# Optimization experiments

Hardware: AMD Instinct MI355X
Metric: run time of the kernel (lower is better)

The kernel has to match this reference:

```python
import jax, jax.numpy as jnp
import numpy as np

EPS = 1e-12
ETA = 1.0


def _l2norm(x, eps=EPS):
    # torch F.normalize: x / max(||x||, eps)
    n = jnp.sqrt(jnp.sum(x * x, axis=-1, keepdims=True))
    return x / jnp.maximum(n, eps)


def setup_inputs() -> dict:
    key = jax.random.key(0)
    ks = jax.random.split(key, 7)
    B, IN, H = 256, 512, 512
    std = 1.0 / np.sqrt(H)
    return {
        "inputs": jax.random.normal(ks[0], (B, IN), jnp.float32),
        "hidden": jax.random.normal(ks[1], (B, H), jnp.float32),
        "assoc_mem": jax.random.normal(ks[2], (B, H, H), jnp.float32),
        "W_ih": jax.random.uniform(ks[3], (3 * H, IN), jnp.float32, -std, std),
        "b_ih": jax.random.uniform(ks[4], (3 * H,), jnp.float32, -std, std),
        "W_hh": jax.random.uniform(ks[5], (3 * H, H), jnp.float32, -std, std),
        "b_hh": jax.random.uniform(ks[6], (3 * H,), jnp.float32, -std, std),
    }


def reference(inputs, hidden, assoc_mem, W_ih, b_ih, W_hh, b_hh):
    H = hidden.shape[-1]
    # projections = ih(inputs) + hh(hidden)  -> [B, 3H]
    proj = inputs @ W_ih.T + b_ih + hidden @ W_hh.T + b_hh
    u_gate, r, x_emb = jnp.split(proj, 3, axis=1)

    # rotation_operator(x_emb, r): Householder-style rotation in span{u, v}
    u = _l2norm(x_emb)                                    # [B, H]
    r_n = _l2norm(r)
    costh = jnp.sum(u * r_n, axis=-1, keepdims=True)      # [B, 1]
    sinth = jnp.sqrt(1.0 - costh ** 2)                    # [B, 1]
    v = _l2norm(r - jnp.sum(u * r, axis=-1, keepdims=True) * u)

    # R = I - uu^T - vv^T + tmp^T Rth tmp
    #   = I + (cos-1)(uu^T + vv^T) + sin (v u^T - u v^T)
    uu = jnp.einsum('bi,bj->bij', u, u)
    vv = jnp.einsum('bi,bj->bij', v, v)
    cross = jnp.einsum('bi,bj->bij', v, u) - jnp.einsum('bi,bj->bij', u, v)
    R = (jnp.eye(H, dtype=hidden.dtype)
         + (costh - 1.0)[..., None] * (uu + vv)
         + sinth[..., None] * cross)                      # [B, H, H]

    # Rth = assoc_mem @ R ; hidden_new = Rth @ hidden
    Rth_full = jnp.einsum('bij,bjk->bik', assoc_mem, R)
    hidden_new = jnp.einsum('bij,bj->bi', Rth_full, hidden)

    c = jax.nn.relu(hidden_new + x_emb)
    new_h = u_gate * hidden + (1.0 - u_gate) * c
    new_h = _l2norm(new_h) * ETA
    return new_h
```

## Files before the change

kernel.cpp:

```cpp
#include <hip/hip_runtime.h>


#define EPSF 1e-12f

__device__ __forceinline__ float block_reduce_sum(float v, float* sbuf) {
#pragma unroll
    for (int off = 32; off >= 1; off >>= 1)
        v += __shfl_xor(v, off, 64);
    const int t = threadIdx.x;
    __syncthreads();
    if ((t & 63) == 0) sbuf[t >> 6] = v;
    __syncthreads();
    return sbuf[0] + sbuf[1] + sbuf[2] + sbuf[3];
}

#define BM 32
#define BN 64
#define BK 32
#define XS_STRIDE (BM + 2)

__global__ __launch_bounds__(256) void gemm_proj(
    const float* __restrict__ inp, const float* __restrict__ hid,
    const float* __restrict__ W_ih, const float* __restrict__ W_hh,
    const float* __restrict__ b_ih, const float* __restrict__ b_hh,
    float* __restrict__ proj)
{
    __shared__ float Xs[BK * XS_STRIDE];
    __shared__ float Ws[BK * BN];
    const int t  = threadIdx.x;
    const int tx = t & 15;
    const int ty = t >> 4;
    const int col0 = blockIdx.x * BN;
    const int row0 = blockIdx.y * BM;

    const int lr = t >> 3;
    const int lk = (t & 7) * 4;

    float acc[2][4] = {};

#pragma unroll
    for (int phase = 0; phase < 2; ++phase) {
        const float* Xg = phase ? hid : inp;
        const float* Wg = phase ? W_hh : W_ih;
        for (int k0 = 0; k0 < 512; k0 += BK) {
            float4 xv  = *(const float4*)(Xg + (size_t)(row0 + lr) * 512 + k0 + lk);
            float4 wv0 = *(const float4*)(Wg + (size_t)(col0 + lr) * 512 + k0 + lk);
            float4 wv1 = *(const float4*)(Wg + (size_t)(col0 + lr + 32) * 512 + k0 + lk);
            __syncthreads();
            Xs[(lk + 0) * XS_STRIDE + lr] = xv.x;
            Xs[(lk + 1) * XS_STRIDE + lr] = xv.y;
            Xs[(lk + 2) * XS_STRIDE + lr] = xv.z;
            Xs[(lk + 3) * XS_STRIDE + lr] = xv.w;
            Ws[(lk + 0) * BN + lr] = wv0.x;
            Ws[(lk + 1) * BN + lr] = wv0.y;
            Ws[(lk + 2) * BN + lr] = wv0.z;
            Ws[(lk + 3) * BN + lr] = wv0.w;
            Ws[(lk + 0) * BN + lr + 32] = wv1.x;
            Ws[(lk + 1) * BN + lr + 32] = wv1.y;
            Ws[(lk + 2) * BN + lr + 32] = wv1.z;
            Ws[(lk + 3) * BN + lr + 32] = wv1.w;
            __syncthreads();
#pragma unroll
            for (int kk = 0; kk < BK; ++kk) {
                float2 xv2 = *(const float2*)&Xs[kk * XS_STRIDE + 2 * ty];
                float4 wv4 = *(const float4*)&Ws[kk * BN + 4 * tx];
                acc[0][0] += xv2.x * wv4.x;
                acc[0][1] += xv2.x * wv4.y;
                acc[0][2] += xv2.x * wv4.z;
                acc[0][3] += xv2.x * wv4.w;
                acc[1][0] += xv2.y * wv4.x;
                acc[1][1] += xv2.y * wv4.y;
                acc[1][2] += xv2.y * wv4.z;
                acc[1][3] += xv2.y * wv4.w;
            }
        }
    }

    const float4 bi = *(const float4*)(b_ih + col0 + 4 * tx);
    const float4 bh = *(const float4*)(b_hh + col0 + 4 * tx);
    const float4 bias = { bi.x + bh.x, bi.y + bh.y, bi.z + bh.z, bi.w + bh.w };
#pragma unroll
    for (int i = 0; i < 2; ++i) {
        const int r = row0 + 2 * ty + i;
        float4 o = { acc[i][0] + bias.x, acc[i][1] + bias.y,
                     acc[i][2] + bias.z, acc[i][3] + bias.w };
        *(float4*)(proj + (size_t)r * 1536 + col0 + 4 * tx) = o;
    }
}

__global__ __launch_bounds__(256) void rotate_kernel(
    const float* __restrict__ proj, const float* __restrict__ hid,
    float* __restrict__ Rh)
{
    __shared__ float sbuf[4];
    const int b = blockIdx.x;
    const int t = threadIdx.x;
    const int j = 2 * t;
    const float* prow = proj + (size_t)b * 1536;
    const float2 x2 = *(const float2*)(prow + 1024 + j);
    const float2 r2 = *(const float2*)(prow + 512 + j);
    const float2 h2 = *(const float2*)(hid + (size_t)b * 512 + j);

    float sx2 = block_reduce_sum(x2.x * x2.x + x2.y * x2.y, sbuf);
    float sr2 = block_reduce_sum(r2.x * r2.x + r2.y * r2.y, sbuf);
    float sxr = block_reduce_sum(x2.x * r2.x + x2.y * r2.y, sbuf);
    float sxh = block_reduce_sum(x2.x * h2.x + x2.y * h2.y, sbuf);

    const float nx = fmaxf(sqrtf(sx2), EPSF);
    const float nr = fmaxf(sqrtf(sr2), EPSF);
    const float costh = sxr / (nx * nr);
    const float sinth = sqrtf(fmaxf(1.0f - costh * costh, 0.0f));
    const float dot_ur = sxr / nx;
    const float a = sxh / nx;

    const float ux = x2.x / nx, uy = x2.y / nx;
    const float wx = r2.x - dot_ur * ux, wy = r2.y - dot_ur * uy;

    float sw2 = block_reduce_sum(wx * wx + wy * wy, sbuf);
    float swh = block_reduce_sum(wx * h2.x + wy * h2.y, sbuf);
    const float nw = fmaxf(sqrtf(sw2), EPSF);
    const float bb = swh / nw;

    const float cm1 = costh - 1.0f;
    const float vx = wx / nw, vy = wy / nw;
    float2 o;
    o.x = h2.x + cm1 * (a * ux + bb * vx) + sinth * (a * vx - bb * ux);
    o.y = h2.y + cm1 * (a * uy + bb * vy) + sinth * (a * vy - bb * uy);
    *(float2*)(Rh + (size_t)b * 512 + j) = o;
}

__global__ __launch_bounds__(256) void matvec_kernel(
    const float* __restrict__ A, const float* __restrict__ Rh,
    float* __restrict__ hn)
{
    __shared__ float Rhs[512];
    const int b = blockIdx.y;
    const int g = blockIdx.x;
    const int t = threadIdx.x;
    *(float2*)(Rhs + 2 * t) = *(const float2*)(Rh + (size_t)b * 512 + 2 * t);
    __syncthreads();
    const int wave = t >> 6, lane = t & 63;
    const float4* Rhs4 = (const float4*)Rhs;
    const float4 x0 = Rhs4[lane];
    const float4 x1 = Rhs4[64 + lane];
    float res = 0.0f;
#pragma unroll 4
    for (int rr = 0; rr < 16; ++rr) {
        const int i = g * 64 + wave * 16 + rr;
        const float4* Arow = (const float4*)(A + ((size_t)b * 512 + i) * 512);
        const float4 a0 = Arow[lane];
        const float4 a1 = Arow[64 + lane];
        float acc = a0.x * x0.x + a0.y * x0.y + a0.z * x0.z + a0.w * x0.w
                  + a1.x * x1.x + a1.y * x1.y + a1.z * x1.z + a1.w * x1.w;
#pragma unroll
        for (int off = 32; off >= 1; off >>= 1)
            acc += __shfl_xor(acc, off, 64);
        if (lane == rr) res = acc;
    }
    if (lane < 16)
        hn[(size_t)b * 512 + g * 64 + wave * 16 + lane] = res;
}

__global__ __launch_bounds__(256) void epilogue_kernel(
    const float* __restrict__ proj, const float* __restrict__ hid,
    const float* __restrict__ hn, float* __restrict__ out)
{
    __shared__ float sbuf[4];
    const int b = blockIdx.x;
    const int t = threadIdx.x;
    const int j = 2 * t;
    const float* prow = proj + (size_t)b * 1536;
    const float2 ug = *(const float2*)(prow + j);
    const float2 xe = *(const float2*)(prow + 1024 + j);
    const float2 h2 = *(const float2*)(hid + (size_t)b * 512 + j);
    const float2 hv = *(const float2*)(hn + (size_t)b * 512 + j);

    const float cx = fmaxf(hv.x + xe.x, 0.0f);
    const float cy = fmaxf(hv.y + xe.y, 0.0f);
    const float tx_ = ug.x * h2.x + (1.0f - ug.x) * cx;
    const float ty_ = ug.y * h2.y + (1.0f - ug.y) * cy;

    const float s = block_reduce_sum(tx_ * tx_ + ty_ * ty_, sbuf);
    const float inv = 1.0f / fmaxf(sqrtf(s), EPSF);
    float2 o = { tx_ * inv, ty_ * inv };
    *(float2*)(out + (size_t)b * 512 + j) = o;
}

extern "C" void kernel_launch(void* const* d_in, const int* in_sizes, int n_in,
                              void* d_out, int out_size, void* d_ws, size_t ws_size,
                              hipStream_t stream)
{
    const float* inp  = (const float*)d_in[0];
    const float* hid  = (const float*)d_in[1];
    const float* A    = (const float*)d_in[2];
    const float* W_ih = (const float*)d_in[3];
    const float* b_ih = (const float*)d_in[4];
    const float* W_hh = (const float*)d_in[5];
    const float* b_hh = (const float*)d_in[6];
    float* out = (float*)d_out;

    float* proj = (float*)d_ws;
    float* Rh   = proj + 256 * 1536;
    float* hn   = Rh + 256 * 512;

    gemm_proj<<<dim3(24, 8), 256, 0, stream>>>(inp, hid, W_ih, W_hh, b_ih, b_hh, proj);
    rotate_kernel<<<dim3(256), 256, 0, stream>>>(proj, hid, Rh);
    matvec_kernel<<<dim3(8, 256), 256, 0, stream>>>(A, Rh, hn);
    epilogue_kernel<<<dim3(256), 256, 0, stream>>>(proj, hid, hn, out);
}
```

Measured before the change: 423.6 us.

## Fuse rotate, matvec and epilogue into one per-batch kernel; prefetch GEMM tiles

Merges the rotation, the batched matrix-vector product over assoc_mem and the normalisation epilogue into a single 1024-thread block per batch row. Rh and hn now stay in shared memory, and the six scalar block reductions are packed into float4 reductions. The matvec reads A with nontemporal loads and 16-lane row groups. The projection GEMM also register-prefetches the next K tile before the compute loop. This removes two launches and the global round-trips of Rh and hn, but only 256 blocks stream the 256 MB matrix, which may limit memory-level parallelism compared with the 2048-block matvec.

Result: faster. 385.8 us (-8.9%).

```diff
diff --git a/kernel.cpp b/kernel.cpp
--- a/kernel.cpp
+++ b/kernel.cpp
@@ -3,21 +3,7 @@
 
 #define EPSF 1e-12f
 
-__device__ __forceinline__ float block_reduce_sum(float v, float* sbuf) {
-#pragma unroll
-    for (int off = 32; off >= 1; off >>= 1)
-        v += __shfl_xor(v, off, 64);
-    const int t = threadIdx.x;
-    __syncthreads();
-    if ((t & 63) == 0) sbuf[t >> 6] = v;
-    __syncthreads();
-    return sbuf[0] + sbuf[1] + sbuf[2] + sbuf[3];
-}
-
-#define BM 32
-#define BN 64
-#define BK 32
-#define XS_STRIDE (BM + 2)
+typedef float vfloat4 __attribute__((ext_vector_type(4)));
 
 __global__ __launch_bounds__(256) void gemm_proj(
     const float* __restrict__ inp, const float* __restrict__ hid,
@@ -25,54 +11,58 @@
     const float* __restrict__ b_ih, const float* __restrict__ b_hh,
     float* __restrict__ proj)
 {
-    __shared__ float Xs[BK * XS_STRIDE];
-    __shared__ float Ws[BK * BN];
+    __shared__ float Xs[32 * 34];
+    __shared__ float Ws[32 * 64];
     const int t  = threadIdx.x;
     const int tx = t & 15;
     const int ty = t >> 4;
-    const int col0 = blockIdx.x * BN;
-    const int row0 = blockIdx.y * BM;
-
+    const int col0 = blockIdx.x * 64;
+    const int row0 = blockIdx.y * 32;
     const int lr = t >> 3;
     const int lk = (t & 7) * 4;
 
     float acc[2][4] = {};
 
-#pragma unroll
-    for (int phase = 0; phase < 2; ++phase) {
-        const float* Xg = phase ? hid : inp;
-        const float* Wg = phase ? W_hh : W_ih;
-        for (int k0 = 0; k0 < 512; k0 += BK) {
-            float4 xv  = *(const float4*)(Xg + (size_t)(row0 + lr) * 512 + k0 + lk);
-            float4 wv0 = *(const float4*)(Wg + (size_t)(col0 + lr) * 512 + k0 + lk);
-            float4 wv1 = *(const float4*)(Wg + (size_t)(col0 + lr + 32) * 512 + k0 + lk);
-            __syncthreads();
-            Xs[(lk + 0) * XS_STRIDE + lr] = xv.x;
-            Xs[(lk + 1) * XS_STRIDE + lr] = xv.y;
-            Xs[(lk + 2) * XS_STRIDE + lr] = xv.z;
-            Xs[(lk + 3) * XS_STRIDE + lr] = xv.w;
-            Ws[(lk + 0) * BN + lr] = wv0.x;
-            Ws[(lk + 1) * BN + lr] = wv0.y;
-            Ws[(lk + 2) * BN + lr] = wv0.z;
-            Ws[(lk + 3) * BN + lr] = wv0.w;
-            Ws[(lk + 0) * BN + lr + 32] = wv1.x;
-            Ws[(lk + 1) * BN + lr + 32] = wv1.y;
-            Ws[(lk + 2) * BN + lr + 32] = wv1.z;
-            Ws[(lk + 3) * BN + lr + 32] = wv1.w;
-            __syncthreads();
-#pragma unroll
-            for (int kk = 0; kk < BK; ++kk) {
-                float2 xv2 = *(const float2*)&Xs[kk * XS_STRIDE + 2 * ty];
-                float4 wv4 = *(const float4*)&Ws[kk * BN + 4 * tx];
-                acc[0][0] += xv2.x * wv4.x;
-                acc[0][1] += xv2.x * wv4.y;
-                acc[0][2] += xv2.x * wv4.z;
-                acc[0][3] += xv2.x * wv4.w;
-                acc[1][0] += xv2.y * wv4.x;
-                acc[1][1] += xv2.y * wv4.y;
-                acc[1][2] += xv2.y * wv4.z;
-                acc[1][3] += xv2.y * wv4.w;
-            }
+    float4 xv  = *(const float4*)(inp  + (size_t)(row0 + lr) * 512 + lk);
+    float4 wv0 = *(const float4*)(W_ih + (size_t)(col0 + lr) * 512 + lk);
+    float4 wv1 = *(const float4*)(W_ih + (size_t)(col0 + lr + 32) * 512 + lk);
+
+    for (int cc = 0; cc < 32; ++cc) {
+        __syncthreads();
+        Xs[(lk + 0) * 34 + lr] = xv.x;
+        Xs[(lk + 1) * 34 + lr] = xv.y;
+        Xs[(lk + 2) * 34 + lr] = xv.z;
+        Xs[(lk + 3) * 34 + lr] = xv.w;
+        Ws[(lk + 0) * 64 + lr] = wv0.x;
+        Ws[(lk + 1) * 64 + lr] = wv0.y;
+        Ws[(lk + 2) * 64 + lr] = wv0.z;
+        Ws[(lk + 3) * 64 + lr] = wv0.w;
+        Ws[(lk + 0) * 64 + lr + 32] = wv1.x;
+        Ws[(lk + 1) * 64 + lr + 32] = wv1.y;
+        Ws[(lk + 2) * 64 + lr + 32] = wv1.z;
+        Ws[(lk + 3) * 64 + lr + 32] = wv1.w;
+
+        const int nc = (cc < 31) ? cc + 1 : 31;
+        const float* Xg = (nc & 16) ? hid  : inp;
+        const float* Wg = (nc & 16) ? W_hh : W_ih;
+        const int k0 = (nc & 15) * 32;
+        xv  = *(const float4*)(Xg + (size_t)(row0 + lr) * 512 + k0 + lk);
+        wv0 = *(const float4*)(Wg + (size_t)(col0 + lr) * 512 + k0 + lk);
+        wv1 = *(const float4*)(Wg + (size_t)(col0 + lr + 32) * 512 + k0 + lk);
+
+        __syncthreads();
+#pragma unroll
+        for (int kk = 0; kk < 32; ++kk) {
+            float2 xv2 = *(const float2*)&Xs[kk * 34 + 2 * ty];
+            float4 wv4 = *(const float4*)&Ws[kk * 64 + 4 * tx];
+            acc[0][0] += xv2.x * wv4.x;
+            acc[0][1] += xv2.x * wv4.y;
+            acc[0][2] += xv2.x * wv4.z;
+            acc[0][3] += xv2.x * wv4.w;
+            acc[1][0] += xv2.y * wv4.x;
+            acc[1][1] += xv2.y * wv4.y;
+            acc[1][2] += xv2.y * wv4.z;
+            acc[1][3] += xv2.y * wv4.w;
         }
     }
 
@@ -88,102 +78,112 @@
     }
 }
 
-__global__ __launch_bounds__(256) void rotate_kernel(
+
+__device__ __forceinline__ float4 block_reduce4_1024(float4 v, float4* red, int t) {
+    __syncthreads();
+#pragma unroll
+    for (int off = 32; off >= 1; off >>= 1) {
+        v.x += __shfl_xor(v.x, off, 64);
+        v.y += __shfl_xor(v.y, off, 64);
+        v.z += __shfl_xor(v.z, off, 64);
+        v.w += __shfl_xor(v.w, off, 64);
+    }
+    if ((t & 63) == 0) red[t >> 6] = v;
+    __syncthreads();
+    float4 s = {0.f, 0.f, 0.f, 0.f};
+#pragma unroll
+    for (int i = 0; i < 16; ++i) {
+        float4 r = red[i];
+        s.x += r.x; s.y += r.y; s.z += r.z; s.w += r.w;
+    }
+    return s;
+}
+
+__global__ __launch_bounds__(1024) void rum_fused(
     const float* __restrict__ proj, const float* __restrict__ hid,
-    float* __restrict__ Rh)
+    const float* __restrict__ A, float* __restrict__ out)
 {
-    __shared__ float sbuf[4];
+    __shared__ float4 Rh4[128];
+    __shared__ float  hn[512];
+    __shared__ float4 red[16];
+    float* Rh = (float*)Rh4;
+
     const int b = blockIdx.x;
     const int t = threadIdx.x;
-    const int j = 2 * t;
     const float* prow = proj + (size_t)b * 1536;
-    const float2 x2 = *(const float2*)(prow + 1024 + j);
-    const float2 r2 = *(const float2*)(prow + 512 + j);
-    const float2 h2 = *(const float2*)(hid + (size_t)b * 512 + j);
-
-    float sx2 = block_reduce_sum(x2.x * x2.x + x2.y * x2.y, sbuf);
-    float sr2 = block_reduce_sum(r2.x * r2.x + r2.y * r2.y, sbuf);
-    float sxr = block_reduce_sum(x2.x * r2.x + x2.y * r2.y, sbuf);
-    float sxh = block_reduce_sum(x2.x * h2.x + x2.y * h2.y, sbuf);
-
-    const float nx = fmaxf(sqrtf(sx2), EPSF);
-    const float nr = fmaxf(sqrtf(sr2), EPSF);
-    const float costh = sxr / (nx * nr);
+
+    float xe = 0.f, rr = 0.f, hh = 0.f;
+    if (t < 512) {
+        xe = prow[1024 + t];
+        rr = prow[512 + t];
+        hh = hid[(size_t)b * 512 + t];
+    }
+    float4 p1 = { xe * xe, rr * rr, xe * rr, xe * hh };
+    p1 = block_reduce4_1024(p1, red, t);
+    const float nx = fmaxf(sqrtf(p1.x), EPSF);
+    const float nr = fmaxf(sqrtf(p1.y), EPSF);
+    const float costh = p1.z / (nx * nr);
     const float sinth = sqrtf(fmaxf(1.0f - costh * costh, 0.0f));
-    const float dot_ur = sxr / nx;
-    const float a = sxh / nx;
-
-    const float ux = x2.x / nx, uy = x2.y / nx;
-    const float wx = r2.x - dot_ur * ux, wy = r2.y - dot_ur * uy;
-
-    float sw2 = block_reduce_sum(wx * wx + wy * wy, sbuf);
-    float swh = block_reduce_sum(wx * h2.x + wy * h2.y, sbuf);
-    const float nw = fmaxf(sqrtf(sw2), EPSF);
-    const float bb = swh / nw;
-
+    const float dot_ur = p1.z / nx;
+    const float a = p1.w / nx;
+    const float u = xe / nx;
+    const float w = rr - dot_ur * u;
+
+    float4 p2 = { w * w, w * hh, 0.f, 0.f };
+    p2 = block_reduce4_1024(p2, red, t);
+    const float nw = fmaxf(sqrtf(p2.x), EPSF);
+    const float bb = p2.y / nw;
+    const float v = w / nw;
     const float cm1 = costh - 1.0f;
-    const float vx = wx / nw, vy = wy / nw;
-    float2 o;
-    o.x = h2.x + cm1 * (a * ux + bb * vx) + sinth * (a * vx - bb * ux);
-    o.y = h2.y + cm1 * (a * uy + bb * vy) + sinth * (a * vy - bb * uy);
-    *(float2*)(Rh + (size_t)b * 512 + j) = o;
-}
-
-__global__ __launch_bounds__(256) void matvec_kernel(
-    const float* __restrict__ A, const float* __restrict__ Rh,
-    float* __restrict__ hn)
-{
-    __shared__ float Rhs[512];
-    const int b = blockIdx.y;
-    const int g = blockIdx.x;
-    const int t = threadIdx.x;
-    *(float2*)(Rhs + 2 * t) = *(const float2*)(Rh + (size_t)b * 512 + 2 * t);
-    __syncthreads();
-    const int wave = t >> 6, lane = t & 63;
-    const float4* Rhs4 = (const float4*)Rhs;
-    const float4 x0 = Rhs4[lane];
-    const float4 x1 = Rhs4[64 + lane];
-    float res = 0.0f;
-#pragma unroll 4
-    for (int rr = 0; rr < 16; ++rr) {
-        const int i = g * 64 + wave * 16 + rr;
-        const float4* Arow = (const float4*)(A + ((size_t)b * 512 + i) * 512);
-        const float4 a0 = Arow[lane];
-        const float4 a1 = Arow[64 + lane];
-        float acc = a0.x * x0.x + a0.y * x0.y + a0.z * x0.z + a0.w * x0.w
-                  + a1.x * x1.x + a1.y * x1.y + a1.z * x1.z + a1.w * x1.w;
-#pragma unroll
-        for (int off = 32; off >= 1; off >>= 1)
-            acc += __shfl_xor(acc, off, 64);
-        if (lane == rr) res = acc;
-    }
-    if (lane < 16)
-        hn[(size_t)b * 512 + g * 64 + wave * 16 + lane] = res;
-}
-
-__global__ __launch_bounds__(256) void epilogue_kernel(
-    const float* __restrict__ proj, const float* __restrict__ hid,
-    const float* __restrict__ hn, float* __restrict__ out)
-{
-    __shared__ float sbuf[4];
-    const int b = blockIdx.x;
-    const int t = threadIdx.x;
-    const int j = 2 * t;
-    const float* prow = proj + (size_t)b * 1536;
-    const float2 ug = *(const float2*)(prow + j);
-    const float2 xe = *(const float2*)(prow + 1024 + j);
-    const float2 h2 = *(const float2*)(hid + (size_t)b * 512 + j);
-    const float2 hv = *(const float2*)(hn + (size_t)b * 512 + j);
-
-    const float cx = fmaxf(hv.x + xe.x, 0.0f);
-    const float cy = fmaxf(hv.y + xe.y, 0.0f);
-    const float tx_ = ug.x * h2.x + (1.0f - ug.x) * cx;
-    const float ty_ = ug.y * h2.y + (1.0f - ug.y) * cy;
-
-    const float s = block_reduce_sum(tx_ * tx_ + ty_ * ty_, sbuf);
-    const float inv = 1.0f / fmaxf(sqrtf(s), EPSF);
-    float2 o = { tx_ * inv, ty_ * inv };
-    *(float2*)(out + (size_t)b * 512 + j) = o;
+    if (t < 512)
+        Rh[t] = hh + cm1 * (a * u + bb * v) + sinth * (a * v - bb * u);
+    __syncthreads();
+
+    const int lane = t & 63;
+    const int wv = t >> 6;
+    const int g = lane >> 4;
+    const int c = lane & 15;
+
+    float4 xr[8];
+#pragma unroll
+    for (int k = 0; k < 8; ++k) xr[k] = Rh4[c + 16 * k];
+
+    const vfloat4* Ab = (const vfloat4*)(A + (size_t)b * 512 * 512);
+#pragma unroll 2
+    for (int q = 0; q < 8; ++q) {
+        const int i = 32 * wv + 4 * q + g;
+        const vfloat4* Ar = Ab + (size_t)i * 128;
+        float a0 = 0.f, a1 = 0.f, a2 = 0.f, a3 = 0.f;
+#pragma unroll
+        for (int k = 0; k < 8; k += 4) {
+            vfloat4 v0 = __builtin_nontemporal_load(Ar + c + 16 * (k + 0));
+            vfloat4 v1 = __builtin_nontemporal_load(Ar + c + 16 * (k + 1));
+            vfloat4 v2 = __builtin_nontemporal_load(Ar + c + 16 * (k + 2));
+            vfloat4 v3 = __builtin_nontemporal_load(Ar + c + 16 * (k + 3));
+            a0 += v0.x * xr[k + 0].x + v0.y * xr[k + 0].y + v0.z * xr[k + 0].z + v0.w * xr[k + 0].w;
+            a1 += v1.x * xr[k + 1].x + v1.y * xr[k + 1].y + v1.z * xr[k + 1].z + v1.w * xr[k + 1].w;
+            a2 += v2.x * xr[k + 2].x + v2.y * xr[k + 2].y + v2.z * xr[k + 2].z + v2.w * xr[k + 2].w;
+            a3 += v3.x * xr[k + 3].x + v3.y * xr[k + 3].y + v3.z * xr[k + 3].z + v3.w * xr[k + 3].w;
+        }
+        float accq = (a0 + a1) + (a2 + a3);
+#pragma unroll
+        for (int off = 8; off >= 1; off >>= 1)
+            accq += __shfl_xor(accq, off, 16);
+        if (c == 0) hn[i] = accq;
+    }
+    __syncthreads();
+
+    float tv = 0.f, ug = 0.f;
+    if (t < 512) {
+        ug = prow[t];
+        const float cx = fmaxf(hn[t] + xe, 0.0f);
+        tv = ug * hh + (1.0f - ug) * cx;
+    }
+    float4 p3 = { tv * tv, 0.f, 0.f, 0.f };
+    p3 = block_reduce4_1024(p3, red, t);
+    const float inv = 1.0f / fmaxf(sqrtf(p3.x), EPSF);
+    if (t < 512)
+        out[(size_t)b * 512 + t] = tv * inv;
 }
 
 extern "C" void kernel_launch(void* const* d_in, const int* in_sizes, int n_in,
@@ -200,11 +200,7 @@
     float* out = (float*)d_out;
 
     float* proj = (float*)d_ws;
-    float* Rh   = proj + 256 * 1536;
-    float* hn   = Rh + 256 * 512;
 
     gemm_proj<<<dim3(24, 8), 256, 0, stream>>>(inp, hid, W_ih, W_hh, b_ih, b_hh, proj);
-    rotate_kernel<<<dim3(256), 256, 0, stream>>>(proj, hid, Rh);
-    matvec_kernel<<<dim3(8, 256), 256, 0, stream>>>(A, Rh, hn);
-    epilogue_kernel<<<dim3(256), 256, 0, stream>>>(proj, hid, hn, out);
-}
+    rum_fused<<<dim3(256), 1024, 0, stream>>>(proj, hid, A, out);
+}
```
